# Performance work log

Measured on AMD Instinct MI355X. Metric: run time of the kernel, lower is better.

Reference implementation:

```python
import jax, jax.numpy as jnp
import numpy as np

B, O, K, GS = 4096, 11008, 4096, 128  # batch, out_features, in_features, group_size
G = K // GS  # num groups = 32


def _unpack_int4(packed):
    """packed: [N, K//2] int values in [0,256) holding two 4-bit nibbles (low first).
    Returns signed int4 values as float32 [N, K]."""
    low = packed & 15
    high = (packed >> 4) & 15
    q = jnp.stack([low, high], axis=-1).reshape(packed.shape[0], -1)  # interleave low,high
    return jnp.where(q >= 8, q - 16, q).astype(jnp.float32)


def setup_inputs() -> dict:
    key = jax.random.key(0)
    k1, k2, k3, k4, k5 = jax.random.split(key, 5)
    x = jax.random.randint(k1, (B, K // 2), 0, 256, dtype=jnp.int32)
    a_scale = jax.random.uniform(k2, (B, G), dtype=jnp.float32).astype(jnp.float16)
    w_packed = jax.random.randint(k3, (O, K // 2), 0, 256, dtype=jnp.int32)
    w_scale = jax.random.uniform(k4, (O, G), dtype=jnp.float32).astype(jnp.float16)
    bias = (jax.random.normal(k5, (O,), dtype=jnp.float32) * 0.02).astype(jnp.float16)
    return {"x": x, "a_scale": a_scale, "w_packed": w_packed, "w_scale": w_scale,
            "bias": bias, "group_size": GS}


def reference(x, a_scale, w_packed, w_scale, bias, group_size):
    # out[b,o] = sum_g a_scale[b,g] * w_scale[o,g] * sum_{k in g} x_int4[b,k] * w_int4[o,k] + bias[o]
    # Fold the per-group scales into the dequantized operands, then a single GEMM
    # (mathematically identical to group-wise int accumulate + dequant).
    b, o = x.shape[0], w_packed.shape[0]
    k = x.shape[1] * 2
    g = k // group_size
    xq = _unpack_int4(x).reshape(b, g, group_size) * a_scale.astype(jnp.float32)[:, :, None]
    wq = _unpack_int4(w_packed).reshape(o, g, group_size) * w_scale.astype(jnp.float32)[:, :, None]
    out = jnp.einsum('bgk,ogk->bo', xq, wq).astype(jnp.float16)  # [B, O] fp16
    return out + bias
```

## Files before the change

### kernel.cpp

```cpp
#include <hip/hip_runtime.h>
#include <hip/hip_bf16.h>


#define B_DIM 4096
#define O_DIM 11008
#define K_DIM 4096
#define G_NUM 32

#define NX32 8388608u
#define NW32 22544384u
#define X8_BYTES  16777216u
#define W8_BYTES  45088768u

typedef int   i32x4 __attribute__((ext_vector_type(4)));
typedef float f32x4 __attribute__((ext_vector_type(4)));

__device__ __forceinline__ unsigned pack2(int v) {
    int t = v ^ 0x88;
    unsigned lo = (unsigned)(((t & 15) - 8) & 0xFF);
    unsigned hi = (unsigned)((((t >> 4) & 15) - 8) & 0xFF);
    return lo | (hi << 8);
}

__global__ __launch_bounds__(256)
void unpack_kernel(const int* __restrict__ xq, const int* __restrict__ wq,
                   unsigned char* __restrict__ X8, unsigned char* __restrict__ W8) {
    unsigned t = blockIdx.x * 256u + threadIdx.x;
    const int* src;
    unsigned char* dst;
    if (t < NX32 / 8) {
        src = xq + (size_t)t * 8;
        dst = X8 + (size_t)t * 16;
    } else {
        unsigned j = t - NX32 / 8;
        src = wq + (size_t)j * 8;
        dst = W8 + (size_t)j * 16;
    }
    int4 v0 = ((const int4*)src)[0];
    int4 v1 = ((const int4*)src)[1];
    uint4 o;
    o.x = pack2(v0.x) | (pack2(v0.y) << 16);
    o.y = pack2(v0.z) | (pack2(v0.w) << 16);
    o.z = pack2(v1.x) | (pack2(v1.y) << 16);
    o.w = pack2(v1.z) | (pack2(v1.w) << 16);
    *(uint4*)dst = o;
}

__global__ __launch_bounds__(256)
void tscale_kernel(const float* __restrict__ as_, const float* __restrict__ ws_,
                   float* __restrict__ asT, float* __restrict__ wsT) {
    int bx = blockIdx.x, g = blockIdx.y, t = threadIdx.x;
    if (bx < 16) {
        int b = bx * 256 + t;
        asT[g * B_DIM + b] = as_[(size_t)b * G_NUM + g];
    } else {
        int o = (bx - 16) * 256 + t;
        wsT[(size_t)g * O_DIM + o] = ws_[(size_t)o * G_NUM + g];
    }
}

__global__ __launch_bounds__(256, 2)
void gemm_i8(const unsigned char* __restrict__ X8, const unsigned char* __restrict__ W8,
             const float* __restrict__ asT, const float* __restrict__ wsT,
             const float* __restrict__ bias, float* __restrict__ out) {
    __shared__ __align__(16) unsigned char A0[16384];
    __shared__ __align__(16) unsigned char B0[16384];
    __shared__ __align__(16) unsigned char A1[16384];
    __shared__ __align__(16) unsigned char B1[16384];

    const int tid  = threadIdx.x;
    const int wv   = tid >> 6;
    const int lane = tid & 63;
    const int quad = lane >> 4;
    const int lq   = lane & 15;
    const int bm   = blockIdx.x;
    const int bn   = blockIdx.y;
    const int wm   = (wv & 1) << 6;
    const int wn   = (wv >> 1) << 6;

    f32x4 facc[4][4] = {};

    const int l8 = lane >> 3;
    const int c8 = lane & 7;
    const int sw_chunk = ((c8 ^ l8) << 4);
    const size_t xrow0 = (size_t)(bm * 128) * K_DIM;
    const size_t wrow0 = (size_t)(bn * 128) * K_DIM;

    auto stage = [&](int g, unsigned char* Ad, unsigned char* Bd) {
        const int gb = g << 7;
#pragma unroll
        for (int s = 0; s < 4; ++s) {
            const int slab = (wv << 2) + s;
            const int row  = (slab << 3) + l8;
            const unsigned char* gpA = X8 + xrow0 + (size_t)row * K_DIM + gb + sw_chunk;
            const unsigned char* gpB = W8 + wrow0 + (size_t)row * K_DIM + gb + sw_chunk;
            __builtin_amdgcn_global_load_lds(
                (const __attribute__((address_space(1))) void*)gpA,
                (__attribute__((address_space(3))) void*)(Ad + (slab << 10)), 16, 0, 0);
            __builtin_amdgcn_global_load_lds(
                (const __attribute__((address_space(1))) void*)gpB,
                (__attribute__((address_space(3))) void*)(Bd + (slab << 10)), 16, 0, 0);
        }
    };

    auto compute = [&](int g, const unsigned char* Ab, const unsigned char* Bb) {
        f32x4 asr[4];
        float wsn[4];
#pragma unroll
        for (int i = 0; i < 4; ++i)
            asr[i] = *(const f32x4*)&asT[(g << 12) + bm * 128 + wm + (i << 4) + (quad << 2)];
#pragma unroll
        for (int j = 0; j < 4; ++j)
            wsn[j] = wsT[(size_t)g * O_DIM + bn * 128 + wn + (j << 4) + lq];

        i32x4 gacc[4][4] = {};
#pragma unroll
        for (int ks = 0; ks < 2; ++ks) {
            i32x4 av[4], bv[4];
            const int pa = ((((ks << 2) + quad) ^ (lq & 7)) << 4);
#pragma unroll
            for (int i = 0; i < 4; ++i) {
                av[i] = *(const i32x4*)&Ab[((wm + (i << 4) + lq) << 7) + pa];
                bv[i] = *(const i32x4*)&Bb[((wn + (i << 4) + lq) << 7) + pa];
            }
#pragma unroll
            for (int i = 0; i < 4; ++i)
#pragma unroll
                for (int j = 0; j < 4; ++j)
                    gacc[i][j] = __builtin_amdgcn_mfma_i32_16x16x64_i8(av[i], bv[j], gacc[i][j], 0, 0, 0);
        }
#pragma unroll
        for (int i = 0; i < 4; ++i)
#pragma unroll
            for (int j = 0; j < 4; ++j)
#pragma unroll
                for (int r = 0; r < 4; ++r)
                    facc[i][j][r] = __builtin_fmaf(asr[i][r] * wsn[j], (float)gacc[i][j][r], facc[i][j][r]);
    };

    stage(0, A0, B0);

    for (int g2 = 0; g2 < G_NUM; g2 += 2) {
        __syncthreads();
        stage(g2 + 1, A1, B1);
        compute(g2, A0, B0);

        __syncthreads();
        if (g2 + 2 < G_NUM) stage(g2 + 2, A0, B0);
        compute(g2 + 1, A1, B1);
    }

    const int n0 = bn * 128 + wn + lq;
    const int m0 = bm * 128 + wm + (quad << 2);
    float bvs[4];
#pragma unroll
    for (int j = 0; j < 4; ++j) bvs[j] = bias[n0 + (j << 4)];
#pragma unroll
    for (int i = 0; i < 4; ++i) {
#pragma unroll
        for (int r = 0; r < 4; ++r) {
            float* orow = out + (size_t)(m0 + (i << 4) + r) * O_DIM;
#pragma unroll
            for (int j = 0; j < 4; ++j)
                orow[n0 + (j << 4)] = facc[i][j][r] + bvs[j];
        }
    }
}

extern "C" void kernel_launch(void* const* d_in, const int* in_sizes, int n_in,
                              void* d_out, int out_size, void* d_ws, size_t ws_size,
                              hipStream_t stream) {
    const int*   xq   = (const int*)d_in[0];
    const float* as_  = (const float*)d_in[1];
    const int*   wq   = (const int*)d_in[2];
    const float* ws_  = (const float*)d_in[3];
    const float* bias = (const float*)d_in[4];
    float* out        = (float*)d_out;

    unsigned char* X8 = (unsigned char*)d_ws;
    unsigned char* W8 = X8 + X8_BYTES;
    float* asT = (float*)((unsigned char*)d_ws + X8_BYTES + W8_BYTES);
    float* wsT = asT + (size_t)G_NUM * B_DIM;

    unpack_kernel<<<(NX32 + NW32) / 8 / 256, 256, 0, stream>>>(xq, wq, X8, W8);
    tscale_kernel<<<dim3(59, 32), 256, 0, stream>>>(as_, ws_, asT, wsT);
    gemm_i8<<<dim3(B_DIM / 128, O_DIM / 128), 256, 0, stream>>>(X8, W8, asT, wsT, bias, out);
}
```

Baseline: 520.5 us.

## Hand-schedule GEMM pipeline with split staging, XCD-aware tile mapping, tiled scale transpose

Rewrites the int8 MFMA main loop so that next-group A/B staging and scale loads are interleaved with the LDS reads and MFMAs, using explicit vmcnt/lgkmcnt waits, one s_barrier per group, sched_barrier and setprio. This replaces the two __syncthreads per pair of groups and prefetches scales one group ahead. The block grid is linearised and remapped so that each XCD handles a contiguous band of M tiles, which is meant to improve L2 reuse of the A rows. The scale transpose kernel now goes through a shared-memory tile with vectorised loads and stores. The hand-counted waitcnt values are fragile and could race if the compiler emits a different number of memory operations.

```diff
diff --git a/kernel.cpp b/kernel.cpp
--- a/kernel.cpp
+++ b/kernel.cpp
@@ -1,5 +1,4 @@
 #include <hip/hip_runtime.h>
-#include <hip/hip_bf16.h>
 
 
 #define B_DIM 4096
@@ -49,13 +48,29 @@
 __global__ __launch_bounds__(256)
 void tscale_kernel(const float* __restrict__ as_, const float* __restrict__ ws_,
                    float* __restrict__ asT, float* __restrict__ wsT) {
-    int bx = blockIdx.x, g = blockIdx.y, t = threadIdx.x;
-    if (bx < 16) {
-        int b = bx * 256 + t;
-        asT[g * B_DIM + b] = as_[(size_t)b * G_NUM + g];
-    } else {
-        int o = (bx - 16) * 256 + t;
-        wsT[(size_t)g * O_DIM + o] = ws_[(size_t)o * G_NUM + g];
+    __shared__ float tile[64][33];
+    const int blk = blockIdx.x, t = threadIdx.x;
+    const float* src; float* dst; int R0, RTOT;
+    if (blk < 64) { src = as_; dst = asT; R0 = blk * 64;        RTOT = B_DIM; }
+    else          { src = ws_; dst = wsT; R0 = (blk - 64) * 64; RTOT = O_DIM; }
+
+    {
+        const int r = t >> 2, cc = (t & 3) * 8;
+        const float* p = src + (size_t)(R0 + r) * G_NUM + cc;
+        f32x4 v0 = *(const f32x4*)p;
+        f32x4 v1 = *(const f32x4*)(p + 4);
+#pragma unroll
+        for (int k = 0; k < 4; ++k) { tile[r][cc + k] = v0[k]; tile[r][cc + 4 + k] = v1[k]; }
+    }
+    __syncthreads();
+    {
+        const int g = t >> 3, bc = (t & 7) * 8;
+        f32x4 w0, w1;
+#pragma unroll
+        for (int k = 0; k < 4; ++k) { w0[k] = tile[bc + k][g]; w1[k] = tile[bc + 4 + k][g]; }
+        float* q = dst + (size_t)g * RTOT + R0 + bc;
+        *(f32x4*)q = w0;
+        *(f32x4*)(q + 4) = w1;
     }
 }
 
@@ -73,8 +88,12 @@
     const int lane = tid & 63;
     const int quad = lane >> 4;
     const int lq   = lane & 15;
-    const int bm   = blockIdx.x;
-    const int bn   = blockIdx.y;
+
+    const unsigned lin = blockIdx.x;
+    const unsigned xcd = lin & 7u, pos = lin >> 3;
+    const int bn = (int)(pos % 86u);
+    const int bm = (int)((xcd << 2) + pos / 86u);
+
     const int wm   = (wv & 1) << 6;
     const int wn   = (wv >> 1) << 6;
 
@@ -85,69 +104,122 @@
     const int sw_chunk = ((c8 ^ l8) << 4);
     const size_t xrow0 = (size_t)(bm * 128) * K_DIM;
     const size_t wrow0 = (size_t)(bn * 128) * K_DIM;
-
-    auto stage = [&](int g, unsigned char* Ad, unsigned char* Bd) {
+    const int abase = bm * 128 + wm + (quad << 2);
+    const int wbase = bn * 128 + wn + lq;
+    const int pa0 = ((quad ^ (lq & 7)) << 4);
+    const int pa1 = (((4 + quad) ^ (lq & 7)) << 4);
+
+    auto stageA = [&](int g, unsigned char* Ad) {
         const int gb = g << 7;
 #pragma unroll
         for (int s = 0; s < 4; ++s) {
             const int slab = (wv << 2) + s;
             const int row  = (slab << 3) + l8;
-            const unsigned char* gpA = X8 + xrow0 + (size_t)row * K_DIM + gb + sw_chunk;
-            const unsigned char* gpB = W8 + wrow0 + (size_t)row * K_DIM + gb + sw_chunk;
+            const unsigned char* gp = X8 + xrow0 + (size_t)row * K_DIM + gb + sw_chunk;
             __builtin_amdgcn_global_load_lds(
-                (const __attribute__((address_space(1))) void*)gpA,
+                (const __attribute__((address_space(1))) void*)gp,
                 (__attribute__((address_space(3))) void*)(Ad + (slab << 10)), 16, 0, 0);
+        }
+    };
+    auto stageB = [&](int g, unsigned char* Bd) {
+        const int gb = g << 7;
+#pragma unroll
+        for (int s = 0; s < 4; ++s) {
+            const int slab = (wv << 2) + s;
+            const int row  = (slab << 3) + l8;
+            const unsigned char* gp = W8 + wrow0 + (size_t)row * K_DIM + gb + sw_chunk;
             __builtin_amdgcn_global_load_lds(
-                (const __attribute__((address_space(1))) void*)gpB,
+                (const __attribute__((address_space(1))) void*)gp,
                 (__attribute__((address_space(3))) void*)(Bd + (slab << 10)), 16, 0, 0);
         }
     };
-
-    auto compute = [&](int g, const unsigned char* Ab, const unsigned char* Bb) {
-        f32x4 asr[4];
-        float wsn[4];
-#pragma unroll
-        for (int i = 0; i < 4; ++i)
-            asr[i] = *(const f32x4*)&asT[(g << 12) + bm * 128 + wm + (i << 4) + (quad << 2)];
+    auto loadScales = [&](int g, f32x4 (&asr)[4], float (&wsn)[4]) {
+#pragma unroll
+        for (int i = 0; i < 4; ++i)
+            asr[i] = *(const f32x4*)&asT[(g << 12) + abase + (i << 4)];
 #pragma unroll
         for (int j = 0; j < 4; ++j)
-            wsn[j] = wsT[(size_t)g * O_DIM + bn * 128 + wn + (j << 4) + lq];
-
+            wsn[j] = wsT[(size_t)g * O_DIM + wbase + (j << 4)];
+    };
+
+    f32x4 asrA[4], asrB[4];
+    float wsnA[4], wsnB[4];
+
+    auto body = [&](int g, const unsigned char* Ac, const unsigned char* Bc,
+                    unsigned char* An, unsigned char* Bn,
+                    f32x4 (&asrC)[4], float (&wsnC)[4],
+                    f32x4 (&asrN)[4], float (&wsnN)[4]) {
+        const int gn = (g + 1 < G_NUM) ? g + 1 : G_NUM - 1;
         i32x4 gacc[4][4] = {};
-#pragma unroll
-        for (int ks = 0; ks < 2; ++ks) {
-            i32x4 av[4], bv[4];
-            const int pa = ((((ks << 2) + quad) ^ (lq & 7)) << 4);
-#pragma unroll
-            for (int i = 0; i < 4; ++i) {
-                av[i] = *(const i32x4*)&Ab[((wm + (i << 4) + lq) << 7) + pa];
-                bv[i] = *(const i32x4*)&Bb[((wn + (i << 4) + lq) << 7) + pa];
+        i32x4 av0[4], bv0[4], av1[4], bv1[4];
+
+#pragma unroll
+        for (int i = 0; i < 4; ++i)
+            av0[i] = *(const i32x4*)&Ac[((wm + (i << 4) + lq) << 7) + pa0];
+        stageA(gn, An);
+        asm volatile("s_waitcnt vmcnt(12)" ::: "memory");
+        __builtin_amdgcn_s_barrier();
+        __builtin_amdgcn_sched_barrier(0);
+
+#pragma unroll
+        for (int j = 0; j < 4; ++j)
+            bv0[j] = *(const i32x4*)&Bc[((wn + (j << 4) + lq) << 7) + pa0];
+        stageB(gn, Bn);
+        asm volatile("s_waitcnt lgkmcnt(0)" ::: "memory");
+        __builtin_amdgcn_sched_barrier(0);
+        __builtin_amdgcn_s_setprio(1);
+#pragma unroll
+        for (int i = 0; i < 4; ++i)
+#pragma unroll
+            for (int j = 0; j < 4; ++j)
+                gacc[i][j] = __builtin_amdgcn_mfma_i32_16x16x64_i8(av0[i], bv0[j], gacc[i][j], 0, 0, 0);
+        __builtin_amdgcn_s_setprio(0);
+
+#pragma unroll
+        for (int i = 0; i < 4; ++i)
+            av1[i] = *(const i32x4*)&Ac[((wm + (i << 4) + lq) << 7) + pa1];
+#pragma unroll
+        for (int j = 0; j < 4; ++j)
+            bv1[j] = *(const i32x4*)&Bc[((wn + (j << 4) + lq) << 7) + pa1];
+        loadScales(gn, asrN, wsnN);
+        asm volatile("s_waitcnt lgkmcnt(0)" ::: "memory");
+        __builtin_amdgcn_sched_barrier(0);
+        __builtin_amdgcn_s_setprio(1);
+#pragma unroll
+        for (int i = 0; i < 4; ++i)
+#pragma unroll
+            for (int j = 0; j < 4; ++j)
+                gacc[i][j] = __builtin_amdgcn_mfma_i32_16x16x64_i8(av1[i], bv1[j], gacc[i][j], 0, 0, 0);
+        __builtin_amdgcn_s_setprio(0);
+
+        asm volatile("s_waitcnt vmcnt(16)" ::: "memory");
+        __builtin_amdgcn_sched_barrier(0);
+#pragma unroll
+        for (int i = 0; i < 4; ++i)
+#pragma unroll
+            for (int j = 0; j < 4; ++j) {
+                f32x4 s = asrC[i] * wsnC[j];
+                f32x4 gf;
+#pragma unroll
+                for (int r = 0; r < 4; ++r) gf[r] = (float)gacc[i][j][r];
+                facc[i][j] += gf * s;
             }
-#pragma unroll
-            for (int i = 0; i < 4; ++i)
-#pragma unroll
-                for (int j = 0; j < 4; ++j)
-                    gacc[i][j] = __builtin_amdgcn_mfma_i32_16x16x64_i8(av[i], bv[j], gacc[i][j], 0, 0, 0);
-        }
-#pragma unroll
-        for (int i = 0; i < 4; ++i)
-#pragma unroll
-            for (int j = 0; j < 4; ++j)
-#pragma unroll
-                for (int r = 0; r < 4; ++r)
-                    facc[i][j][r] = __builtin_fmaf(asr[i][r] * wsn[j], (float)gacc[i][j][r], facc[i][j][r]);
-    };
-
-    stage(0, A0, B0);
-
+        asm volatile("s_waitcnt vmcnt(12)" ::: "memory");
+        __builtin_amdgcn_s_barrier();
+        __builtin_amdgcn_sched_barrier(0);
+    };
+
+    stageA(0, A0);
+    stageB(0, B0);
+    loadScales(0, asrA, wsnA);
+    asm volatile("s_waitcnt vmcnt(12)" ::: "memory");
+    __builtin_amdgcn_s_barrier();
+    __builtin_amdgcn_sched_barrier(0);
+
+#pragma unroll 1
     for (int g2 = 0; g2 < G_NUM; g2 += 2) {
-        __syncthreads();
-        stage(g2 + 1, A1, B1);
-        compute(g2, A0, B0);
-
-        __syncthreads();
-        if (g2 + 2 < G_NUM) stage(g2 + 2, A0, B0);
-        compute(g2 + 1, A1, B1);
+        body(g2,     A0, B0, A1, B1, asrA, wsnA, asrB, wsnB);
+        body(g2 + 1, A1, B1, A0, B0, asrB, wsnB, asrA, wsnA);
     }
 
     const int n0 = bn * 128 + wn + lq;
@@ -183,6 +255,6 @@
     float* wsT = asT + (size_t)G_NUM * B_DIM;
 
     unpack_kernel<<<(NX32 + NW32) / 8 / 256, 256, 0, stream>>>(xq, wq, X8, W8);
-    tscale_kernel<<<dim3(59, 32), 256, 0, stream>>>(as_, ws_, asT, wsT);
-    gemm_i8<<<dim3(B_DIM / 128, O_DIM / 128), 256, 0, stream>>>(X8, W8, asT, wsT, bias, out);
-}
+    tscale_kernel<<<64 + 172, 256, 0, stream>>>(as_, ws_, asT, wsT);
+    gemm_i8<<<dim3((B_DIM / 128) * (O_DIM / 128)), 256, 0, stream>>>(X8, W8, asT, wsT, bias, out);
+}
```

Result: slower. 561.4 us (+7.9%).

## Restructure MFMA inner loop per A-row with register prefetch; tile scale transpose

Applied to the files above, without the earlier changes.

The group compute is reorganized so each A row-tile's MFMA results are dequantized and accumulated right away, instead of holding a full 4x4 int32 accumulator array. This lowers register pressure, and the next A fragment is prefetched from LDS while the current MFMAs run. The scale-transpose kernel now goes through a shared-memory tile with vectorized loads and stores instead of strided scalar accesses. The risk is a shorter dependency chain between each MFMA result and its conversion, which can stall the pipeline.

```diff
diff --git a/kernel.cpp b/kernel.cpp
--- a/kernel.cpp
+++ b/kernel.cpp
@@ -1,5 +1,4 @@
 #include <hip/hip_runtime.h>
-#include <hip/hip_bf16.h>
 
 
 #define B_DIM 4096
@@ -49,13 +48,28 @@
 __global__ __launch_bounds__(256)
 void tscale_kernel(const float* __restrict__ as_, const float* __restrict__ ws_,
                    float* __restrict__ asT, float* __restrict__ wsT) {
-    int bx = blockIdx.x, g = blockIdx.y, t = threadIdx.x;
-    if (bx < 16) {
-        int b = bx * 256 + t;
-        asT[g * B_DIM + b] = as_[(size_t)b * G_NUM + g];
-    } else {
-        int o = (bx - 16) * 256 + t;
-        wsT[(size_t)g * O_DIM + o] = ws_[(size_t)o * G_NUM + g];
+    __shared__ float tile[64][33];
+    const int blk = blockIdx.x, t = threadIdx.x;
+    const float* src; float* dst; int R0, RTOT;
+    if (blk < 64) { src = as_; dst = asT; R0 = blk * 64;        RTOT = B_DIM; }
+    else          { src = ws_; dst = wsT; R0 = (blk - 64) * 64; RTOT = O_DIM; }
+    {
+        const int r = t >> 2, cc = (t & 3) * 8;
+        const float* p = src + (size_t)(R0 + r) * G_NUM + cc;
+        f32x4 v0 = *(const f32x4*)p;
+        f32x4 v1 = *(const f32x4*)(p + 4);
+#pragma unroll
+        for (int k = 0; k < 4; ++k) { tile[r][cc + k] = v0[k]; tile[r][cc + 4 + k] = v1[k]; }
+    }
+    __syncthreads();
+    {
+        const int g = t >> 3, bc = (t & 7) * 8;
+        f32x4 w0, w1;
+#pragma unroll
+        for (int k = 0; k < 4; ++k) { w0[k] = tile[bc + k][g]; w1[k] = tile[bc + 4 + k][g]; }
+        float* q = dst + (size_t)g * RTOT + R0 + bc;
+        *(f32x4*)q = w0;
+        *(f32x4*)(q + 4) = w1;
     }
 }
 
@@ -85,6 +99,10 @@
     const int sw_chunk = ((c8 ^ l8) << 4);
     const size_t xrow0 = (size_t)(bm * 128) * K_DIM;
     const size_t wrow0 = (size_t)(bn * 128) * K_DIM;
+    const int abase = bm * 128 + wm + (quad << 2);
+    const int wbase = bn * 128 + wn + lq;
+    const int pa0 = ((quad ^ (lq & 7)) << 4);
+    const int pa1 = (((4 + quad) ^ (lq & 7)) << 4);
 
     auto stage = [&](int g, unsigned char* Ad, unsigned char* Bd) {
         const int gb = g << 7;
@@ -108,34 +126,43 @@
         float wsn[4];
 #pragma unroll
         for (int i = 0; i < 4; ++i)
-            asr[i] = *(const f32x4*)&asT[(g << 12) + bm * 128 + wm + (i << 4) + (quad << 2)];
+            asr[i] = *(const f32x4*)&asT[(g << 12) + abase + (i << 4)];
 #pragma unroll
         for (int j = 0; j < 4; ++j)
-            wsn[j] = wsT[(size_t)g * O_DIM + bn * 128 + wn + (j << 4) + lq];
-
-        i32x4 gacc[4][4] = {};
-#pragma unroll
-        for (int ks = 0; ks < 2; ++ks) {
-            i32x4 av[4], bv[4];
-            const int pa = ((((ks << 2) + quad) ^ (lq & 7)) << 4);
-#pragma unroll
-            for (int i = 0; i < 4; ++i) {
-                av[i] = *(const i32x4*)&Ab[((wm + (i << 4) + lq) << 7) + pa];
-                bv[i] = *(const i32x4*)&Bb[((wn + (i << 4) + lq) << 7) + pa];
+            wsn[j] = wsT[(size_t)g * O_DIM + wbase + (j << 4)];
+
+        i32x4 bv0[4], bv1[4];
+#pragma unroll
+        for (int j = 0; j < 4; ++j) {
+            bv0[j] = *(const i32x4*)&Bb[((wn + (j << 4) + lq) << 7) + pa0];
+            bv1[j] = *(const i32x4*)&Bb[((wn + (j << 4) + lq) << 7) + pa1];
+        }
+        i32x4 a0c = *(const i32x4*)&Ab[((wm + lq) << 7) + pa0];
+        i32x4 a1c = *(const i32x4*)&Ab[((wm + lq) << 7) + pa1];
+
+#pragma unroll
+        for (int i = 0; i < 4; ++i) {
+            const i32x4 a0 = a0c, a1 = a1c;
+            if (i < 3) {
+                a0c = *(const i32x4*)&Ab[((wm + ((i + 1) << 4) + lq) << 7) + pa0];
+                a1c = *(const i32x4*)&Ab[((wm + ((i + 1) << 4) + lq) << 7) + pa1];
             }
-#pragma unroll
-            for (int i = 0; i < 4; ++i)
-#pragma unroll
-                for (int j = 0; j < 4; ++j)
-                    gacc[i][j] = __builtin_amdgcn_mfma_i32_16x16x64_i8(av[i], bv[j], gacc[i][j], 0, 0, 0);
-        }
-#pragma unroll
-        for (int i = 0; i < 4; ++i)
+            i32x4 q[4];
 #pragma unroll
             for (int j = 0; j < 4; ++j)
-#pragma unroll
-                for (int r = 0; r < 4; ++r)
-                    facc[i][j][r] = __builtin_fmaf(asr[i][r] * wsn[j], (float)gacc[i][j][r], facc[i][j][r]);
+                q[j] = __builtin_amdgcn_mfma_i32_16x16x64_i8(a0, bv0[j], (i32x4){0, 0, 0, 0}, 0, 0, 0);
+#pragma unroll
+            for (int j = 0; j < 4; ++j)
+                q[j] = __builtin_amdgcn_mfma_i32_16x16x64_i8(a1, bv1[j], q[j], 0, 0, 0);
+#pragma unroll
+            for (int j = 0; j < 4; ++j) {
+                const f32x4 s = asr[i] * wsn[j];
+                f32x4 gf;
+#pragma unroll
+                for (int r = 0; r < 4; ++r) gf[r] = (float)q[j][r];
+                facc[i][j] += gf * s;
+            }
+        }
     };
 
     stage(0, A0, B0);
@@ -183,6 +210,6 @@
     float* wsT = asT + (size_t)G_NUM * B_DIM;
 
     unpack_kernel<<<(NX32 + NW32) / 8 / 256, 256, 0, stream>>>(xq, wq, X8, W8);
-    tscale_kernel<<<dim3(59, 32), 256, 0, stream>>>(as_, ws_, asT, wsT);
+    tscale_kernel<<<64 + 172, 256, 0, stream>>>(as_, ws_, asT, wsT);
     gemm_i8<<<dim3(B_DIM / 128, O_DIM / 128), 256, 0, stream>>>(X8, W8, asT, wsT, bias, out);
 }
```

Measured after the change: 523.9 us. Within noise of the previous version (+0.6%).
